# Optimization experiments

Measured on AMD Instinct MI355X. Metric: run time of the kernel, lower is better.

## Reference

```python
import jax, jax.numpy as jnp
import numpy as np

L = 8192   # residues / nodes
E = 524288 # contact-map edges (avg degree 64)
NEG_SLOPE = 0.2  # PyG GATConv default negative_slope


def gat_layer(x, src, dst, Wg, asrc, adst, bias):
    """PyG-style GATConv (v1), concat heads, eval mode (no dropout).
    x: [L, F_in]; Wg: [F_in, H*C]; asrc/adst: [H, C]; bias: [H*C]."""
    H, C = asrc.shape
    h = (x @ Wg).reshape(L, H, C)                      # [L,H,C]
    a_s = jnp.einsum('nhc,hc->nh', h, asrc)            # [L,H]
    a_d = jnp.einsum('nhc,hc->nh', h, adst)            # [L,H]
    e = jax.nn.leaky_relu(a_s[src] + a_d[dst], NEG_SLOPE)  # [E',H]
    # softmax over incoming edges of each destination node
    m = jax.ops.segment_max(e, dst, num_segments=L)
    ex = jnp.exp(e - m[dst])
    denom = jax.ops.segment_sum(ex, dst, num_segments=L)
    alpha = ex / (denom[dst] + 1e-16)                  # [E',H]
    msg = h[src] * alpha[:, :, None]                   # [E',H,C]
    out = jax.ops.segment_sum(msg, dst, num_segments=L)  # [L,H,C]
    return out.reshape(L, H * C) + bias


def setup_inputs() -> dict:
    key = jax.random.key(0)
    ks = jax.random.split(key, 16)
    def g(k, shape, scale=0.05):
        return (jax.random.normal(k, shape, dtype=jnp.float32) * scale)
    return {
        'input_seq': jax.random.normal(ks[0], (1, L, 26), dtype=jnp.float32),
        'edge_index': jax.random.randint(ks[1], (2, E), 0, L, dtype=jnp.int32),
        'W1': g(ks[2], (26, 1024)),
        'W2': g(ks[3], (1024, 256)),
        'Wg1': g(ks[4], (256, 256)),
        'asrc1': g(ks[5], (4, 64)),
        'adst1': g(ks[6], (4, 64)),
        'b1': g(ks[7], (256,)),
        'Wg2': g(ks[8], (256, 512)),
        'asrc2': g(ks[9], (4, 128)),
        'adst2': g(ks[10], (4, 128)),
        'b2': g(ks[11], (512,)),
        'fcW': g(ks[12], (512, 512)),
        'fcb': g(ks[13], (512,)),
        'outW': g(ks[14], (512, 489)),
        'outb': g(ks[15], (489,)),
    }


def reference(input_seq, edge_index, W1, W2, Wg1, asrc1, adst1, b1,
              Wg2, asrc2, adst2, b2, fcW, fcb, outW, outb):
    # input_layer: Linear(26,1024,no bias) -> ReLU -> Linear(1024,256,no bias)
    x = jax.nn.relu(input_seq[0] @ W1) @ W2            # [L,256]
    # add self-loops (PyG GATConv default)
    loops = jnp.arange(L, dtype=edge_index.dtype)
    src = jnp.concatenate([edge_index[0], loops])
    dst = jnp.concatenate([edge_index[1], loops])
    # two GAT layers with ReLU activation
    x = jax.nn.relu(gat_layer(x, src, dst, Wg1, asrc1, adst1, b1))  # [L,256]
    x = jax.nn.relu(gat_layer(x, src, dst, Wg2, asrc2, adst2, b2))  # [L,512]
    # sum-pool over residues (x.sum(dim=1) with batch=1)
    pooled = x.sum(axis=0, keepdims=True)              # [1,512]
    # fc layers (dropout inactive in eval)
    h = jax.nn.relu(pooled @ fcW + fcb)                # [1,512]
    return h @ outW + outb                             # [1,489]
```

## Files before the change

### kernel.cpp

```cpp
#include <hip/hip_runtime.h>
#include <hip/hip_bf16.h>

constexpr int L = 8192;
constexpr int H = 4;

typedef __attribute__((ext_vector_type(8))) short bf16x8;
typedef __attribute__((ext_vector_type(8))) unsigned short u16x8;
typedef __attribute__((ext_vector_type(4))) float f32x4;

#if defined(__has_builtin)
#  if __has_builtin(__builtin_amdgcn_fdot2_f32_bf16)
#    define HAVE_DOT2 1
#  endif
#endif
#ifndef HAVE_DOT2
#  define HAVE_DOT2 0
#endif
#if HAVE_DOT2
typedef __attribute__((ext_vector_type(2))) __bf16 bfx2;
#endif

static __device__ __forceinline__ float lrelu(float e) {
  return e > 0.f ? e : 0.2f * e;
}
static __device__ __forceinline__ float b2f(unsigned short s) {
  return __uint_as_float(((unsigned)s) << 16);
}
static __device__ __forceinline__ unsigned short f2b(float f) {
  __hip_bfloat16 h = __float2bfloat16(f);
  return *reinterpret_cast<unsigned short*>(&h);
}

template<int PAIRS>
static __device__ __forceinline__ void edge_fma(const unsigned* hv, uint2 m, float* acc) {
#if HAVE_DOT2
#pragma unroll
  for (int p = 0; p < PAIRS; p++) {
    acc[2 * p]     = __builtin_amdgcn_fdot2_f32_bf16(
        __builtin_bit_cast(bfx2, hv[p]), __builtin_bit_cast(bfx2, m.x), acc[2 * p], false);
    acc[2 * p + 1] = __builtin_amdgcn_fdot2_f32_bf16(
        __builtin_bit_cast(bfx2, hv[p]), __builtin_bit_cast(bfx2, m.y), acc[2 * p + 1], false);
  }
#else
  float af = b2f((unsigned short)(m.x & 0xffffu));
#pragma unroll
  for (int p = 0; p < PAIRS; p++) {
    acc[2 * p]     = fmaf(af, b2f((unsigned short)(hv[p] & 0xffffu)), acc[2 * p]);
    acc[2 * p + 1] = fmaf(af, b2f((unsigned short)(hv[p] >> 16)), acc[2 * p + 1]);
  }
#endif
}

__global__ __launch_bounds__(256) void conv_combo(
    const float* __restrict__ seq, const float* __restrict__ W1,
    const float* __restrict__ W2, const float* __restrict__ Wg1,
    const float* __restrict__ Wg2, const float* __restrict__ fcW,
    const float* __restrict__ outW, const int* __restrict__ ei,
    const float* __restrict__ as1, const float* __restrict__ ad1,
    const float* __restrict__ as2, const float* __restrict__ ad2,
    int E, int Etot,
    __hip_bfloat16* __restrict__ xb, __hip_bfloat16* __restrict__ W1t,
    __hip_bfloat16* __restrict__ W2t, __hip_bfloat16* __restrict__ Wg1t,
    __hip_bfloat16* __restrict__ Wg2t, float* __restrict__ fcWt,
    float* __restrict__ outWt, float* __restrict__ wa2,
    int* __restrict__ deg, int* __restrict__ rank) {
  __shared__ float tile[32][33];
  if (blockIdx.x < 992) {
    int b = blockIdx.x;
    const float* src; void* dst; bool obf16; int K, N, Kout, kt, nt;
    if (b < 256)               { src = W2;  dst = W2t;  obf16 = true;  K = 1024; N = 256; Kout = 1024; nt = b & 7;  kt = b >> 3; }
    else if ((b -= 256) < 64)  { src = Wg1; dst = Wg1t; obf16 = true;  K = 256;  N = 256; Kout = 256;  nt = b & 7;  kt = b >> 3; }
    else if ((b -= 64) < 128)  { src = Wg2; dst = Wg2t; obf16 = true;  K = 256;  N = 512; Kout = 256;  nt = b & 15; kt = b >> 4; }
    else if ((b -= 128) < 256) { src = fcW; dst = fcWt; obf16 = false; K = 512;  N = 512; Kout = 512;  nt = b & 15; kt = b >> 4; }
    else if ((b -= 256) < 256) { src = outW;dst = outWt;obf16 = false; K = 512;  N = 489; Kout = 512;  nt = b & 15; kt = b >> 4; }
    else { b -= 256;             src = W1;  dst = W1t;  obf16 = true;  K = 26;   N = 1024;Kout = 32;   nt = b;      kt = 0; }
    int t = threadIdx.x;
    int lr = t >> 3, lc4 = (t & 7) * 4;
    int gk = kt * 32 + lr, gn = nt * 32 + lc4;
    float4 v = {0.f, 0.f, 0.f, 0.f};
    if (gk < K) {
      const float* p = &src[(size_t)gk * N + gn];
      v.x = (gn + 0 < N) ? p[0] : 0.f;
      v.y = (gn + 1 < N) ? p[1] : 0.f;
      v.z = (gn + 2 < N) ? p[2] : 0.f;
      v.w = (gn + 3 < N) ? p[3] : 0.f;
    }
    tile[lr][lc4 + 0] = v.x; tile[lr][lc4 + 1] = v.y;
    tile[lr][lc4 + 2] = v.z; tile[lr][lc4 + 3] = v.w;
    __syncthreads();
    int on = nt * 32 + lr, ok = kt * 32 + lc4;
    if (on >= N || ok >= Kout) return;
    float o0 = tile[lc4 + 0][lr], o1 = tile[lc4 + 1][lr];
    float o2 = tile[lc4 + 2][lr], o3 = tile[lc4 + 3][lr];
    if (obf16) {
      ushort4 u = {f2b(o0), f2b(o1), f2b(o2), f2b(o3)};
      *(ushort4*)&((__hip_bfloat16*)dst)[(size_t)on * Kout + ok] = u;
    } else {
      float4 u = {o0, o1, o2, o3};
      *(float4*)&((float*)dst)[(size_t)on * Kout + ok] = u;
    }
    return;
  }
  int i = (blockIdx.x - 992) * 256 + threadIdx.x;
  if (i < 262144) { int r = i >> 5, k = i & 31;
    xb[i] = __float2bfloat16(k < 26 ? seq[r * 26 + k] : 0.f); return; }
  i -= 262144;
  if (i < 2048) {
    int k = i >> 3, o = i & 7, h = o & 3;
    const float* av = (o < 4) ? as1 : ad1;
    float s = 0.f;
    for (int c = 0; c < 64; c++) s += Wg1[k * 256 + h * 64 + c] * av[h * 64 + c];
    Wg1t[(size_t)(256 + o) * 256 + k] = __float2bfloat16(s); return; }
  i -= 2048;
  if (i < 2048) {
    int k = i >> 3, o = i & 7, h = o & 3;
    const float* av = (o < 4) ? as2 : ad2;
    float s = 0.f;
    for (int c = 0; c < 128; c++) s += Wg2[k * 512 + h * 128 + c] * av[h * 128 + c];
    wa2[i] = s; return; }
  i -= 2048;
  if (i < 14336) {
    ((__hip_bfloat16*)Wg1t)[(size_t)264 * 256 + i] = __float2bfloat16(0.f); return; }
  i -= 14336;
  if (i < Etot) {
    int dst = (i < E) ? ei[E + i] : (i - E);
    rank[i] = atomicAdd(&deg[dst], 1);
  }
}

template<int BK, bool RELU, bool ASD>
__global__ __launch_bounds__(256) void gemm_big(
    const __hip_bfloat16* __restrict__ A, const __hip_bfloat16* __restrict__ Bt,
    __hip_bfloat16* __restrict__ C, float* __restrict__ asd,
    int M, int N, int K) {
  __shared__ __align__(16) short As[128][BK + 8];
  __shared__ __align__(16) short Bs[64][BK + 8];
  int tid = threadIdx.x;
  int m0 = blockIdx.y * 128, n0 = blockIdx.x * 64;
  int w = tid >> 6, lane = tid & 63;
  int wm = (w >> 1) * 64, wn = (w & 1) * 32;
  f32x4 acc[4][2] = {};
  for (int k0 = 0; k0 < K; k0 += BK) {
    if constexpr (BK == 64) {
#pragma unroll
      for (int i = 0; i < 4; i++) {
        int ch = i * 256 + tid; int r = ch >> 3, kg = ch & 7;
        *(bf16x8*)&As[r][kg * 8] = *(const bf16x8*)&A[(size_t)(m0 + r) * K + k0 + kg * 8];
      }
#pragma unroll
      for (int i = 0; i < 2; i++) {
        int ch = i * 256 + tid; int r = ch >> 3, kg = ch & 7;
        *(bf16x8*)&Bs[r][kg * 8] = *(const bf16x8*)&Bt[(size_t)(n0 + r) * K + k0 + kg * 8];
      }
    } else {
#pragma unroll
      for (int i = 0; i < 2; i++) {
        int ch = i * 256 + tid; int r = ch >> 2, kg = ch & 3;
        *(bf16x8*)&As[r][kg * 8] = *(const bf16x8*)&A[(size_t)(m0 + r) * K + k0 + kg * 8];
      }
      { int r = tid >> 2, kg = tid & 3;
        *(bf16x8*)&Bs[r][kg * 8] = *(const bf16x8*)&Bt[(size_t)(n0 + r) * K + k0 + kg * 8]; }
    }
    __syncthreads();
    int kk = (lane >> 4) * 8;
#pragma unroll
    for (int ks = 0; ks < BK / 32; ks++) {
      bf16x8 af[4], bfr[2];
#pragma unroll
      for (int m = 0; m < 4; m++)
        af[m] = *(const bf16x8*)&As[wm + m * 16 + (lane & 15)][ks * 32 + kk];
#pragma unroll
      for (int n = 0; n < 2; n++)
        bfr[n] = *(const bf16x8*)&Bs[wn + n * 16 + (lane & 15)][ks * 32 + kk];
#pragma unroll
      for (int m = 0; m < 4; m++)
#pragma unroll
        for (int n = 0; n < 2; n++)
          acc[m][n] = __builtin_amdgcn_mfma_f32_16x16x32_bf16(af[m], bfr[n], acc[m][n], 0, 0, 0);
    }
    __syncthreads();
  }
#pragma unroll
  for (int m = 0; m < 4; m++) {
#pragma unroll
    for (int n = 0; n < 2; n++) {
      int col = n0 + wn + n * 16 + (lane & 15);
#pragma unroll
      for (int j = 0; j < 4; j++) {
        int row = m0 + wm + m * 16 + (lane >> 4) * 4 + j;
        float v = acc[m][n][j];
        if (RELU) v = fmaxf(v, 0.f);
        if (!ASD) {
          C[(size_t)row * N + col] = __float2bfloat16(v);
        } else {
          if (col < N) C[(size_t)row * N + col] = __float2bfloat16(v);
          else if (col < N + 8) asd[(size_t)row * 8 + (col - N)] = v;
        }
      }
    }
  }
}

__global__ __launch_bounds__(1024) void scan_deg(const int* __restrict__ deg,
                                                 int* __restrict__ row_start,
                                                 float* __restrict__ pooled) {
  __shared__ int wsum[16];
  int t = threadIdx.x;
  if (t < 512) pooled[t] = 0.f;
  int lane = t & 63, w = t >> 6;
  int local[8];
  int sum = 0;
#pragma unroll
  for (int j = 0; j < 8; j++) { local[j] = deg[t * 8 + j]; sum += local[j]; }
  int v = sum;
#pragma unroll
  for (int off = 1; off < 64; off <<= 1) {
    int u = __shfl_up(v, off);
    if (lane >= off) v += u;
  }
  if (lane == 63) wsum[w] = v;
  __syncthreads();
  int woff = 0;
  for (int i = 0; i < w; i++) woff += wsum[i];
  int base = woff + v - sum;
#pragma unroll
  for (int j = 0; j < 8; j++) { row_start[t * 8 + j] = base; base += local[j]; }
  if (t == 1023) row_start[L] = base;
}

__global__ void scatter_edges(const int* __restrict__ ei, int E, int Etot,
                              const int* __restrict__ row_start,
                              const int* __restrict__ rank, int* __restrict__ csr_src) {
  int e = blockIdx.x * blockDim.x + threadIdx.x;
  if (e >= Etot) return;
  int srcv, dstv;
  if (e < E) { srcv = ei[e]; dstv = ei[E + e]; } else { srcv = dstv = e - E; }
  csr_src[row_start[dstv] + rank[e]] = srcv;
}

template<int C, int PHASES, bool ASD2>
__global__ __launch_bounds__(128) void gat_fused(
    const __hip_bfloat16* __restrict__ hfeat, const float* __restrict__ a_sd,
    const int* __restrict__ row_start, const int* __restrict__ csr_src,
    const float* __restrict__ bias, __hip_bfloat16* __restrict__ out,
    const float* __restrict__ wa2, float* __restrict__ a_sd2) {
  constexpr int HC = 4 * C;
  constexpr int VEC = HC / PHASES / 64;
  constexpr int PAIRS = VEC / 2;
  constexpr int BATCH = 12;
  int wid = threadIdx.x >> 6, lane = threadIdx.x & 63;
  int n = blockIdx.x * 2 + wid;
  int c0 = blockIdx.y * 256 + lane * VEC;
  int hh = c0 / C;
  int hl = hh & 3;
  int rs = row_start[n], re = row_start[n + 1];
  float4 ad4 = *(const float4*)&a_sd[(size_t)n * 8 + 4];

  __shared__ __align__(16) uint2 s_m[2][64][4];
  float dp[4] = {0.f, 0.f, 0.f, 0.f};
  float acc[VEC] = {};
  const unsigned short* hbase = (const unsigned short*)hfeat;

  int base = rs;
  int cnt = min(64, re - rs);
  int srcv = 0;
  float4 as4 = {0.f, 0.f, 0.f, 0.f};
  if (lane < cnt) {
    srcv = csr_src[rs + lane];
    as4 = *(const float4*)&a_sd[(size_t)srcv * 8];
  }

  while (base < re) {
    float w0 = 0.f, w1 = 0.f, w2 = 0.f, w3 = 0.f;
    if (lane < cnt) {
      w0 = __expf(lrelu(as4.x + ad4.x));
      w1 = __expf(lrelu(as4.y + ad4.y));
      w2 = __expf(lrelu(as4.z + ad4.z));
      w3 = __expf(lrelu(as4.w + ad4.w));
    }
    dp[0] += w0; dp[1] += w1; dp[2] += w2; dp[3] += w3;
    unsigned l0 = f2b(w0), l1 = f2b(w1), l2 = f2b(w2), l3 = f2b(w3);
    uint4 ma = {l0, l0 << 16, l1, l1 << 16};
    uint4 mb = {l2, l2 << 16, l3, l3 << 16};
    *(uint4*)&s_m[wid][lane][0] = ma;
    *(uint4*)&s_m[wid][lane][2] = mb;
    asm volatile("s_waitcnt lgkmcnt(0)" ::: "memory");
    int cur_src = srcv;
    int cur_cnt = cnt;
    int nbase = base + 64;
    bool have_next = nbase < re;
    cnt = min(64, re - nbase);
    srcv = 0;
    if (have_next && lane < cnt) srcv = csr_src[nbase + lane];
    float4 nas4 = {0.f, 0.f, 0.f, 0.f};
    bool did_asd = false;

    int j = 0;
    for (; j + BATCH <= cur_cnt; j += BATCH) {
      int srs[BATCH];
#pragma unroll
      for (int k = 0; k < BATCH; k++) srs[k] = __builtin_amdgcn_readlane(cur_src, j + k);
      unsigned hv[BATCH][PAIRS];
#pragma unroll
      for (int k = 0; k < BATCH; k++) {
        const unsigned short* hp = &hbase[(size_t)srs[k] * HC + c0];
        *(uint2*)&hv[k][0] = *(const uint2*)hp;
      }
      if (j == 0 && have_next) {
        if (lane < cnt) nas4 = *(const float4*)&a_sd[(size_t)srcv * 8];
        did_asd = true;
      }
#pragma unroll
      for (int k = 0; k < BATCH; k++) {
        uint2 m = s_m[wid][j + k][hl];
        edge_fma<PAIRS>(hv[k], m, acc);
      }
    }
    if (have_next && !did_asd && lane < cnt)
      nas4 = *(const float4*)&a_sd[(size_t)srcv * 8];
    for (; j < cur_cnt; j++) {
      int sr = __builtin_amdgcn_readlane(cur_src, j);
      unsigned hv[PAIRS];
      const unsigned short* hp = &hbase[(size_t)sr * HC + c0];
      *(uint2*)&hv[0] = *(const uint2*)hp;
      uint2 m = s_m[wid][j][hl];
      edge_fma<PAIRS>(hv, m, acc);
    }
    as4 = nas4;
    base = nbase;
  }

#pragma unroll
  for (int off = 32; off > 0; off >>= 1) {
#pragma unroll
    for (int h = 0; h < 4; h++) dp[h] += __shfl_xor(dp[h], off);
  }
  float dsel = hl == 0 ? dp[0] : hl == 1 ? dp[1] : hl == 2 ? dp[2] : dp[3];
  float inv = 1.f / (dsel + 1e-16f);

#pragma unroll
  for (int k = 0; k < VEC; k++)
    acc[k] = fmaxf(fmaf(acc[k], inv, bias[c0 + k]), 0.f);
  unsigned short* op = (unsigned short*)out + (size_t)n * HC + c0;
  ushort4 ov = {f2b(acc[0]), f2b(acc[1]), f2b(acc[2]), f2b(acc[3])};
  *(ushort4*)op = ov;

  if constexpr (ASD2) {
    float p[8] = {};
#pragma unroll
    for (int q = 0; q < VEC; q++) {
      const float* wr = &wa2[(size_t)(c0 + q) * 8];
#pragma unroll
      for (int o = 0; o < 8; o++) p[o] = fmaf(acc[q], wr[o], p[o]);
    }
#pragma unroll
    for (int off = 32; off > 0; off >>= 1) {
#pragma unroll
      for (int o = 0; o < 8; o++) p[o] += __shfl_xor(p[o], off);
    }
    if (lane == 0) {
      float4 p0 = {p[0], p[1], p[2], p[3]};
      float4 p1 = {p[4], p[5], p[6], p[7]};
      *(float4*)&a_sd2[(size_t)n * 8 + 0] = p0;
      *(float4*)&a_sd2[(size_t)n * 8 + 4] = p1;
    }
  }
}

__global__ __launch_bounds__(512) void col_sum_bf16(const __hip_bfloat16* __restrict__ x,
                                                    float* __restrict__ pooled) {
  int t = threadIdx.x;
  float acc = 0.f;
  for (int r = blockIdx.x; r < L; r += 64)
    acc += b2f(*(const unsigned short*)&x[(size_t)r * 512 + t]);
  atomicAdd(&pooled[t], acc);
}

__global__ __launch_bounds__(256) void fc1(const float* __restrict__ pooled,
                                           const float* __restrict__ Wt,
                                           const float* __restrict__ b,
                                           float* __restrict__ out) {
  __shared__ float pv[512];
  __shared__ float red[256];
  int t = threadIdx.x;
  pv[t] = pooled[t]; pv[t + 256] = pooled[t + 256];
  __syncthreads();
  int ol = t >> 4;
  int o = blockIdx.x * 16 + ol;
  int ks = (t & 15) * 32;
  float p = 0.f;
  const float* wr = &Wt[(size_t)o * 512 + ks];
#pragma unroll
  for (int kk = 0; kk < 32; kk++) p = fmaf(pv[ks + kk], wr[kk], p);
  red[t] = p;
  __syncthreads();
  if ((t & 15) == 0) {
    float s2 = 0.f;
#pragma unroll
    for (int i = 0; i < 16; i++) s2 += red[ol * 16 + i];
    out[o] = fmaxf(s2 + b[o], 0.f);
  }
}

__global__ __launch_bounds__(256) void fc2(const float* __restrict__ h,
                                           const float* __restrict__ Wt,
                                           const float* __restrict__ outb,
                                           float* __restrict__ out) {
  __shared__ float pv[512];
  __shared__ float red[256];
  int t = threadIdx.x;
  pv[t] = h[t]; pv[t + 256] = h[t + 256];
  __syncthreads();
  int ol = t >> 4;
  int o = blockIdx.x * 16 + ol;
  int ks = (t & 15) * 32;
  float p = 0.f;
  const float* wr = &Wt[(size_t)o * 512 + ks];
#pragma unroll
  for (int kk = 0; kk < 32; kk++) p = fmaf(pv[ks + kk], wr[kk], p);
  red[t] = p;
  __syncthreads();
  if ((t & 15) == 0 && o < 489) {
    float s2 = 0.f;
#pragma unroll
    for (int i = 0; i < 16; i++) s2 += red[ol * 16 + i];
    out[o] = s2 + outb[o];
  }
}

extern "C" void kernel_launch(void* const* d_in, const int* in_sizes, int n_in,
                              void* d_out, int out_size, void* d_ws, size_t ws_size,
                              hipStream_t stream) {
  const float* seq   = (const float*)d_in[0];
  const int*   ei    = (const int*)d_in[1];
  const float* W1    = (const float*)d_in[2];
  const float* W2    = (const float*)d_in[3];
  const float* Wg1   = (const float*)d_in[4];
  const float* asrc1 = (const float*)d_in[5];
  const float* adst1 = (const float*)d_in[6];
  const float* b1    = (const float*)d_in[7];
  const float* Wg2   = (const float*)d_in[8];
  const float* asrc2 = (const float*)d_in[9];
  const float* adst2 = (const float*)d_in[10];
  const float* b2    = (const float*)d_in[11];
  const float* fcW   = (const float*)d_in[12];
  const float* fcb   = (const float*)d_in[13];
  const float* outW  = (const float*)d_in[14];
  const float* outb  = (const float*)d_in[15];
  float* outp = (float*)d_out;

  const int E = in_sizes[1] / 2;
  const int Etot = E + L;

  char* ws = (char*)d_ws;
  __hip_bfloat16* mlp1 = (__hip_bfloat16*)(ws + 0);
  __hip_bfloat16* out2 = (__hip_bfloat16*)(ws + 0);
  __hip_bfloat16* h2   = (__hip_bfloat16*)(ws + (16u << 20));
  __hip_bfloat16* x0   = (__hip_bfloat16*)(ws + (24u << 20));
  __hip_bfloat16* h1   = (__hip_bfloat16*)(ws + (28u << 20));
  __hip_bfloat16* out1 = (__hip_bfloat16*)(ws + (32u << 20));
  size_t off = (36u << 20);
  __hip_bfloat16* xb   = (__hip_bfloat16*)(ws + off); off += (size_t)L * 32 * 2;
  __hip_bfloat16* W1t  = (__hip_bfloat16*)(ws + off); off += (size_t)1024 * 32 * 2;
  __hip_bfloat16* W2t  = (__hip_bfloat16*)(ws + off); off += (size_t)256 * 1024 * 2;
  __hip_bfloat16* Wg1t = (__hip_bfloat16*)(ws + off); off += (size_t)320 * 256 * 2;
  __hip_bfloat16* Wg2t = (__hip_bfloat16*)(ws + off); off += (size_t)512 * 256 * 2;
  float* fcWt  = (float*)(ws + off); off += (size_t)512 * 512 * 4;
  float* outWt = (float*)(ws + off); off += (size_t)512 * 512 * 4;
  int* csr_src = (int*)(ws + off); off += (size_t)Etot * 4;
  int* rank    = (int*)(ws + off); off += (size_t)Etot * 4;
  off = (off + 255) & ~(size_t)255;
  int* row_start = (int*)(ws + off); off += (size_t)(L + 1) * 4;
  off = (off + 255) & ~(size_t)255;
  int* deg    = (int*)(ws + off); off += (size_t)L * 4;
  float* a_sd1 = (float*)(ws + off); off += (size_t)L * 8 * 4;
  float* a_sd2 = (float*)(ws + off); off += (size_t)L * 8 * 4;
  float* wa2 = (float*)(ws + off); off += 2048 * 4;
  float* pooled = (float*)(ws + off); off += 512 * 4;
  float* hbuf   = (float*)(ws + off); off += 512 * 4;

  hipMemsetAsync(deg, 0, (size_t)L * 4, stream);

  int convN = 262144 + 2048 + 2048 + 14336 + Etot;
  int convB = (convN + 255) / 256;
  conv_combo<<<992 + convB, 256, 0, stream>>>(
      seq, W1, W2, Wg1, Wg2, fcW, outW, ei, asrc1, adst1, asrc2, adst2, E, Etot,
      xb, W1t, W2t, Wg1t, Wg2t, fcWt, outWt, wa2, deg, rank);

  scan_deg<<<1, 1024, 0, stream>>>(deg, row_start, pooled);
  scatter_edges<<<(Etot + 255) / 256, 256, 0, stream>>>(ei, E, Etot, row_start, rank, csr_src);

  gemm_big<32, true, false><<<dim3(16, 64), 256, 0, stream>>>(xb, W1t, mlp1, nullptr, L, 1024, 32);
  gemm_big<64, false, false><<<dim3(4, 64), 256, 0, stream>>>(mlp1, W2t, x0, nullptr, L, 256, 1024);

  gemm_big<64, false, true><<<dim3(5, 64), 256, 0, stream>>>(x0, Wg1t, h1, a_sd1, L, 256, 256);
  gat_fused<64, 1, true><<<dim3(4096, 1), 128, 0, stream>>>(h1, a_sd1, row_start, csr_src, b1, out1, wa2, a_sd2);

  gemm_big<64, false, false><<<dim3(8, 64), 256, 0, stream>>>(out1, Wg2t, h2, nullptr, L, 512, 256);
  gat_fused<128, 2, false><<<dim3(4096, 2), 128, 0, stream>>>(h2, a_sd2, row_start, csr_src, b2, out2, nullptr, nullptr);

  col_sum_bf16<<<64, 512, 0, stream>>>(out2, pooled);
  fc1<<<32, 256, 0, stream>>>(pooled, fcWt, fcb, hbuf);
  fc2<<<31, 256, 0, stream>>>(hbuf, outWt, outb, outp);
}
```

Measured before the change: 220.5 us.

## Split each node's edges across two waves and double-buffer feature gathers

Each GAT block now handles one destination node instead of two, and the node's incoming edges are split between its two waves. The partial accumulators and softmax denominators are combined through shared memory after a block barrier. The gather loop is also restructured into a two-buffer software pipeline with batch 8, so the next batch's loads are issued before the current batch is consumed. This targets per-node latency and load imbalance, at the cost of twice as many blocks, an extra barrier and an LDS reduction, with one wave idle during the epilogue.

```diff
diff --git a/kernel.cpp b/kernel.cpp
--- a/kernel.cpp
+++ b/kernel.cpp
@@ -247,16 +247,21 @@
   constexpr int HC = 4 * C;
   constexpr int VEC = HC / PHASES / 64;
   constexpr int PAIRS = VEC / 2;
-  constexpr int BATCH = 12;
+  constexpr int BATCH = 8;
   int wid = threadIdx.x >> 6, lane = threadIdx.x & 63;
-  int n = blockIdx.x * 2 + wid;
+  int n = blockIdx.x;
   int c0 = blockIdx.y * 256 + lane * VEC;
-  int hh = c0 / C;
-  int hl = hh & 3;
-  int rs = row_start[n], re = row_start[n + 1];
+  int hl = (c0 / C) & 3;
+  int rs0 = row_start[n], re0 = row_start[n + 1];
+  int degn = re0 - rs0;
+  int halfd = (degn + 1) >> 1;
+  int rs = rs0 + wid * halfd;
+  int re = min(re0, rs + halfd);
   float4 ad4 = *(const float4*)&a_sd[(size_t)n * 8 + 4];
 
   __shared__ __align__(16) uint2 s_m[2][64][4];
+  __shared__ float s_acc[64][VEC];
+  __shared__ float s_dp[4];
   float dp[4] = {0.f, 0.f, 0.f, 0.f};
   float acc[VEC] = {};
   const unsigned short* hbase = (const unsigned short*)hfeat;
@@ -293,36 +298,38 @@
     srcv = 0;
     if (have_next && lane < cnt) srcv = csr_src[nbase + lane];
     float4 nas4 = {0.f, 0.f, 0.f, 0.f};
-    bool did_asd = false;
-
-    int j = 0;
-    for (; j + BATCH <= cur_cnt; j += BATCH) {
-      int srs[BATCH];
-#pragma unroll
-      for (int k = 0; k < BATCH; k++) srs[k] = __builtin_amdgcn_readlane(cur_src, j + k);
-      unsigned hv[BATCH][PAIRS];
+
+    unsigned hvA[BATCH][PAIRS], hvB[BATCH][PAIRS];
+    auto issue = [&](unsigned (&hv)[BATCH][PAIRS], int jb) {
 #pragma unroll
       for (int k = 0; k < BATCH; k++) {
-        const unsigned short* hp = &hbase[(size_t)srs[k] * HC + c0];
-        *(uint2*)&hv[k][0] = *(const uint2*)hp;
+        int sr = __builtin_amdgcn_readlane(cur_src, jb + k);
+        *(uint2*)&hv[k][0] = *(const uint2*)&hbase[(size_t)sr * HC + c0];
       }
-      if (j == 0 && have_next) {
-        if (lane < cnt) nas4 = *(const float4*)&a_sd[(size_t)srcv * 8];
-        did_asd = true;
-      }
+    };
+    auto consume = [&](unsigned (&hv)[BATCH][PAIRS], int jb) {
 #pragma unroll
       for (int k = 0; k < BATCH; k++) {
-        uint2 m = s_m[wid][j + k][hl];
+        uint2 m = s_m[wid][jb + k][hl];
         edge_fma<PAIRS>(hv[k], m, acc);
       }
-    }
-    if (have_next && !did_asd && lane < cnt)
+    };
+
+    int j = 0;
+    if (j + BATCH <= cur_cnt) issue(hvA, j);
+    if (have_next && lane < cnt)
       nas4 = *(const float4*)&a_sd[(size_t)srcv * 8];
+    for (; j + 2 * BATCH <= cur_cnt; j += 2 * BATCH) {
+      issue(hvB, j + BATCH);
+      consume(hvA, j);
+      if (j + 3 * BATCH <= cur_cnt) issue(hvA, j + 2 * BATCH);
+      consume(hvB, j + BATCH);
+    }
+    if (j + BATCH <= cur_cnt) { consume(hvA, j); j += BATCH; }
     for (; j < cur_cnt; j++) {
       int sr = __builtin_amdgcn_readlane(cur_src, j);
       unsigned hv[PAIRS];
-      const unsigned short* hp = &hbase[(size_t)sr * HC + c0];
-      *(uint2*)&hv[0] = *(const uint2*)hp;
+      *(uint2*)&hv[0] = *(const uint2*)&hbase[(size_t)sr * HC + c0];
       uint2 m = s_m[wid][j][hl];
       edge_fma<PAIRS>(hv, m, acc);
     }
@@ -335,7 +342,17 @@
 #pragma unroll
     for (int h = 0; h < 4; h++) dp[h] += __shfl_xor(dp[h], off);
   }
-  float dsel = hl == 0 ? dp[0] : hl == 1 ? dp[1] : hl == 2 ? dp[2] : dp[3];
+
+  if (wid == 1) {
+#pragma unroll
+    for (int k = 0; k < VEC; k++) s_acc[lane][k] = acc[k];
+    if (lane == 0) { s_dp[0] = dp[0]; s_dp[1] = dp[1]; s_dp[2] = dp[2]; s_dp[3] = dp[3]; }
+  }
+  __syncthreads();
+  if (wid == 1) return;
+#pragma unroll
+  for (int k = 0; k < VEC; k++) acc[k] += s_acc[lane][k];
+  float dsel = (hl == 0 ? dp[0] : hl == 1 ? dp[1] : hl == 2 ? dp[2] : dp[3]) + s_dp[hl];
   float inv = 1.f / (dsel + 1e-16f);
 
 #pragma unroll
@@ -494,10 +511,10 @@
   gemm_big<64, false, false><<<dim3(4, 64), 256, 0, stream>>>(mlp1, W2t, x0, nullptr, L, 256, 1024);
 
   gemm_big<64, false, true><<<dim3(5, 64), 256, 0, stream>>>(x0, Wg1t, h1, a_sd1, L, 256, 256);
-  gat_fused<64, 1, true><<<dim3(4096, 1), 128, 0, stream>>>(h1, a_sd1, row_start, csr_src, b1, out1, wa2, a_sd2);
+  gat_fused<64, 1, true><<<dim3(L, 1), 128, 0, stream>>>(h1, a_sd1, row_start, csr_src, b1, out1, wa2, a_sd2);
 
   gemm_big<64, false, false><<<dim3(8, 64), 256, 0, stream>>>(out1, Wg2t, h2, nullptr, L, 512, 256);
-  gat_fused<128, 2, false><<<dim3(4096, 2), 128, 0, stream>>>(h2, a_sd2, row_start, csr_src, b2, out2, nullptr, nullptr);
+  gat_fused<128, 2, false><<<dim3(L, 2), 128, 0, stream>>>(h2, a_sd2, row_start, csr_src, b2, out2, nullptr, nullptr);
 
   col_sum_bf16<<<64, 512, 0, stream>>>(out2, pooled);
   fc1<<<32, 256, 0, stream>>>(pooled, fcWt, fcb, hbuf);
```

New measurement: 225.2 us. +2.1%, slower.

## Reorder GAT layer 2 to aggregate before projecting, fusing bias/ReLU/pool into GEMM

Applied to the files above, without the earlier changes.

Layer 2 now aggregates the 256-wide input features per head with attention weights, producing a [L,4,256] tensor, and only then projects each head through its slice of Wg2. This avoids gathering the 512-wide projected features per edge. The projection GEMM adds the bias, applies ReLU and column-sums into pooled via atomics, so the out2 tensor and the separate col_sum kernel go away. The trade-off is a larger intermediate (1024 columns per node) and four times more GEMM work per head. The attention logits a_sd2 still come from the fused layer-1 kernel.

```diff
diff --git a/kernel.cpp b/kernel.cpp
--- a/kernel.cpp
+++ b/kernel.cpp
@@ -201,6 +201,78 @@
   }
 }
 
+__global__ __launch_bounds__(256) void gemm_head(
+    const __hip_bfloat16* __restrict__ agg,
+    const __hip_bfloat16* __restrict__ Wg2t,
+    const float* __restrict__ b2,
+    float* __restrict__ pooled) {
+  constexpr int BK = 64;
+  __shared__ __align__(16) short As[128][BK + 8];
+  __shared__ __align__(16) short Bs[64][BK + 8];
+  __shared__ float s_cs[4][32];
+  int tid = threadIdx.x;
+  int z = blockIdx.z;
+  int m0 = blockIdx.y * 128, n0 = blockIdx.x * 64;
+  const __hip_bfloat16* A = agg + (size_t)z * 256;
+  const __hip_bfloat16* Bt = Wg2t + (size_t)z * 128 * 256;
+  int w = tid >> 6, lane = tid & 63;
+  int wm = (w >> 1) * 64, wn = (w & 1) * 32;
+  f32x4 acc[4][2] = {};
+  for (int k0 = 0; k0 < 256; k0 += BK) {
+#pragma unroll
+    for (int i = 0; i < 4; i++) {
+      int ch = i * 256 + tid; int r = ch >> 3, kg = ch & 7;
+      *(bf16x8*)&As[r][kg * 8] = *(const bf16x8*)&A[(size_t)(m0 + r) * 1024 + k0 + kg * 8];
+    }
+#pragma unroll
+    for (int i = 0; i < 2; i++) {
+      int ch = i * 256 + tid; int r = ch >> 3, kg = ch & 7;
+      *(bf16x8*)&Bs[r][kg * 8] = *(const bf16x8*)&Bt[(size_t)(n0 + r) * 256 + k0 + kg * 8];
+    }
+    __syncthreads();
+    int kk = (lane >> 4) * 8;
+#pragma unroll
+    for (int ks = 0; ks < BK / 32; ks++) {
+      bf16x8 af[4], bfr[2];
+#pragma unroll
+      for (int m = 0; m < 4; m++)
+        af[m] = *(const bf16x8*)&As[wm + m * 16 + (lane & 15)][ks * 32 + kk];
+#pragma unroll
+      for (int n = 0; n < 2; n++)
+        bfr[n] = *(const bf16x8*)&Bs[wn + n * 16 + (lane & 15)][ks * 32 + kk];
+#pragma unroll
+      for (int m = 0; m < 4; m++)
+#pragma unroll
+        for (int n = 0; n < 2; n++)
+          acc[m][n] = __builtin_amdgcn_mfma_f32_16x16x32_bf16(af[m], bfr[n], acc[m][n], 0, 0, 0);
+    }
+    __syncthreads();
+  }
+  float cs[2] = {0.f, 0.f};
+#pragma unroll
+  for (int n = 0; n < 2; n++) {
+    float bv = b2[z * 128 + n0 + wn + n * 16 + (lane & 15)];
+#pragma unroll
+    for (int m = 0; m < 4; m++)
+#pragma unroll
+      for (int j = 0; j < 4; j++)
+        cs[n] += fmaxf(acc[m][n][j] + bv, 0.f);
+  }
+#pragma unroll
+  for (int n = 0; n < 2; n++) {
+    cs[n] += __shfl_xor(cs[n], 16);
+    cs[n] += __shfl_xor(cs[n], 32);
+  }
+  if (lane < 16) { s_cs[w][lane] = cs[0]; s_cs[w][16 + lane] = cs[1]; }
+  __syncthreads();
+  if (tid < 64) {
+    int c = tid;
+    int bsel = c >> 5;
+    float s = s_cs[bsel][c & 31] + s_cs[bsel + 2][c & 31];
+    atomicAdd(&pooled[z * 128 + n0 + c], s);
+  }
+}
+
 __global__ __launch_bounds__(1024) void scan_deg(const int* __restrict__ deg,
                                                  int* __restrict__ row_start,
                                                  float* __restrict__ pooled) {
@@ -238,21 +310,20 @@
   csr_src[row_start[dstv] + rank[e]] = srcv;
 }
 
-template<int C, int PHASES, bool ASD2>
+template<int C, bool ASD2>
 __global__ __launch_bounds__(128) void gat_fused(
     const __hip_bfloat16* __restrict__ hfeat, const float* __restrict__ a_sd,
     const int* __restrict__ row_start, const int* __restrict__ csr_src,
     const float* __restrict__ bias, __hip_bfloat16* __restrict__ out,
     const float* __restrict__ wa2, float* __restrict__ a_sd2) {
   constexpr int HC = 4 * C;
-  constexpr int VEC = HC / PHASES / 64;
+  constexpr int VEC = HC / 64;
   constexpr int PAIRS = VEC / 2;
   constexpr int BATCH = 12;
   int wid = threadIdx.x >> 6, lane = threadIdx.x & 63;
   int n = blockIdx.x * 2 + wid;
-  int c0 = blockIdx.y * 256 + lane * VEC;
-  int hh = c0 / C;
-  int hl = hh & 3;
+  int c0 = lane * VEC;
+  int hl = (c0 / C) & 3;
   int rs = row_start[n], re = row_start[n + 1];
   float4 ad4 = *(const float4*)&a_sd[(size_t)n * 8 + 4];
 
@@ -367,13 +438,111 @@
   }
 }
 
-__global__ __launch_bounds__(512) void col_sum_bf16(const __hip_bfloat16* __restrict__ x,
-                                                    float* __restrict__ pooled) {
-  int t = threadIdx.x;
-  float acc = 0.f;
-  for (int r = blockIdx.x; r < L; r += 64)
-    acc += b2f(*(const unsigned short*)&x[(size_t)r * 512 + t]);
-  atomicAdd(&pooled[t], acc);
+__global__ __launch_bounds__(128) void gat_agg(
+    const __hip_bfloat16* __restrict__ feat,
+    const float* __restrict__ a_sd,
+    const int* __restrict__ row_start, const int* __restrict__ csr_src,
+    __hip_bfloat16* __restrict__ agg) {
+  constexpr int BATCH = 8;
+  int wid = threadIdx.x >> 6, lane = threadIdx.x & 63;
+  int n = blockIdx.x * 2 + wid;
+  int c0 = lane * 4;
+  int rs = row_start[n], re = row_start[n + 1];
+  float4 ad4 = *(const float4*)&a_sd[(size_t)n * 8 + 4];
+
+  __shared__ __align__(16) uint2 s_m[2][64][4];
+  float dp[4] = {0.f, 0.f, 0.f, 0.f};
+  float acc[4][4] = {};
+  const unsigned short* hbase = (const unsigned short*)feat;
+
+  int base = rs;
+  int cnt = min(64, re - rs);
+  int srcv = 0;
+  float4 as4 = {0.f, 0.f, 0.f, 0.f};
+  if (lane < cnt) {
+    srcv = csr_src[rs + lane];
+    as4 = *(const float4*)&a_sd[(size_t)srcv * 8];
+  }
+
+  while (base < re) {
+    float w0 = 0.f, w1 = 0.f, w2 = 0.f, w3 = 0.f;
+    if (lane < cnt) {
+      w0 = __expf(lrelu(as4.x + ad4.x));
+      w1 = __expf(lrelu(as4.y + ad4.y));
+      w2 = __expf(lrelu(as4.z + ad4.z));
+      w3 = __expf(lrelu(as4.w + ad4.w));
+    }
+    dp[0] += w0; dp[1] += w1; dp[2] += w2; dp[3] += w3;
+    unsigned l0 = f2b(w0), l1 = f2b(w1), l2 = f2b(w2), l3 = f2b(w3);
+    uint4 ma = {l0, l0 << 16, l1, l1 << 16};
+    uint4 mb = {l2, l2 << 16, l3, l3 << 16};
+    *(uint4*)&s_m[wid][lane][0] = ma;
+    *(uint4*)&s_m[wid][lane][2] = mb;
+    asm volatile("s_waitcnt lgkmcnt(0)" ::: "memory");
+    int cur_src = srcv;
+    int cur_cnt = cnt;
+    int nbase = base + 64;
+    bool have_next = nbase < re;
+    cnt = min(64, re - nbase);
+    srcv = 0;
+    if (have_next && lane < cnt) srcv = csr_src[nbase + lane];
+    float4 nas4 = {0.f, 0.f, 0.f, 0.f};
+    bool did_asd = false;
+
+    int j = 0;
+    for (; j + BATCH <= cur_cnt; j += BATCH) {
+      int srs[BATCH];
+#pragma unroll
+      for (int k = 0; k < BATCH; k++) srs[k] = __builtin_amdgcn_readlane(cur_src, j + k);
+      uint2 hv[BATCH];
+#pragma unroll
+      for (int k = 0; k < BATCH; k++)
+        hv[k] = *(const uint2*)&hbase[(size_t)srs[k] * 256 + c0];
+      if (j == 0 && have_next) {
+        if (lane < cnt) nas4 = *(const float4*)&a_sd[(size_t)srcv * 8];
+        did_asd = true;
+      }
+#pragma unroll
+      for (int k = 0; k < BATCH; k++) {
+        uint4 mA = *(const uint4*)&s_m[wid][j + k][0];
+        uint4 mB = *(const uint4*)&s_m[wid][j + k][2];
+        unsigned hp[2] = {hv[k].x, hv[k].y};
+        edge_fma<2>(hp, uint2{mA.x, mA.y}, acc[0]);
+        edge_fma<2>(hp, uint2{mA.z, mA.w}, acc[1]);
+        edge_fma<2>(hp, uint2{mB.x, mB.y}, acc[2]);
+        edge_fma<2>(hp, uint2{mB.z, mB.w}, acc[3]);
+      }
+    }
+    if (have_next && !did_asd && lane < cnt)
+      nas4 = *(const float4*)&a_sd[(size_t)srcv * 8];
+    for (; j < cur_cnt; j++) {
+      int sr = __builtin_amdgcn_readlane(cur_src, j);
+      uint2 hvv = *(const uint2*)&hbase[(size_t)sr * 256 + c0];
+      uint4 mA = *(const uint4*)&s_m[wid][j][0];
+      uint4 mB = *(const uint4*)&s_m[wid][j][2];
+      unsigned hp[2] = {hvv.x, hvv.y};
+      edge_fma<2>(hp, uint2{mA.x, mA.y}, acc[0]);
+      edge_fma<2>(hp, uint2{mA.z, mA.w}, acc[1]);
+      edge_fma<2>(hp, uint2{mB.x, mB.y}, acc[2]);
+      edge_fma<2>(hp, uint2{mB.z, mB.w}, acc[3]);
+    }
+    as4 = nas4;
+    base = nbase;
+  }
+
+#pragma unroll
+  for (int off = 32; off > 0; off >>= 1) {
+#pragma unroll
+    for (int h = 0; h < 4; h++) dp[h] += __shfl_xor(dp[h], off);
+  }
+  unsigned short* op = (unsigned short*)agg + (size_t)n * 1024 + c0;
+#pragma unroll
+  for (int h = 0; h < 4; h++) {
+    float inv = 1.f / (dp[h] + 1e-16f);
+    ushort4 ov = {f2b(acc[h][0] * inv), f2b(acc[h][1] * inv),
+                  f2b(acc[h][2] * inv), f2b(acc[h][3] * inv)};
+    *(ushort4*)(op + h * 256) = ov;
+  }
 }
 
 __global__ __launch_bounds__(256) void fc1(const float* __restrict__ pooled,
@@ -454,8 +623,7 @@
 
   char* ws = (char*)d_ws;
   __hip_bfloat16* mlp1 = (__hip_bfloat16*)(ws + 0);
-  __hip_bfloat16* out2 = (__hip_bfloat16*)(ws + 0);
-  __hip_bfloat16* h2   = (__hip_bfloat16*)(ws + (16u << 20));
+  __hip_bfloat16* agg2 = (__hip_bfloat16*)(ws + 0);
   __hip_bfloat16* x0   = (__hip_bfloat16*)(ws + (24u << 20));
   __hip_bfloat16* h1   = (__hip_bfloat16*)(ws + (28u << 20));
   __hip_bfloat16* out1 = (__hip_bfloat16*)(ws + (32u << 20));
@@ -494,12 +662,11 @@
   gemm_big<64, false, false><<<dim3(4, 64), 256, 0, stream>>>(mlp1, W2t, x0, nullptr, L, 256, 1024);
 
   gemm_big<64, false, true><<<dim3(5, 64), 256, 0, stream>>>(x0, Wg1t, h1, a_sd1, L, 256, 256);
-  gat_fused<64, 1, true><<<dim3(4096, 1), 128, 0, stream>>>(h1, a_sd1, row_start, csr_src, b1, out1, wa2, a_sd2);
-
-  gemm_big<64, false, false><<<dim3(8, 64), 256, 0, stream>>>(out1, Wg2t, h2, nullptr, L, 512, 256);
-  gat_fused<128, 2, false><<<dim3(4096, 2), 128, 0, stream>>>(h2, a_sd2, row_start, csr_src, b2, out2, nullptr, nullptr);
-
-  col_sum_bf16<<<64, 512, 0, stream>>>(out2, pooled);
+  gat_fused<64, true><<<4096, 128, 0, stream>>>(h1, a_sd1, row_start, csr_src, b1, out1, wa2, a_sd2);
+
+  gat_agg<<<4096, 128, 0, stream>>>(out1, a_sd2, row_start, csr_src, agg2);
+  gemm_head<<<dim3(2, 64, 4), 256, 0, stream>>>(agg2, Wg2t, b2, pooled);
+
   fc1<<<32, 256, 0, stream>>>(pooled, fcWt, fcb, hbuf);
   fc2<<<31, 256, 0, stream>>>(hbuf, outWt, outb, outp);
 }
```

Result: faster. 184.2 us (-16.5%).
